# Optimization experiments

Measured on AMD Instinct MI355X. Metric: run time of the kernel, lower is better.

Reference implementation:

```python
import jax, jax.numpy as jnp
import numpy as np


def dct_mat(N, dtype=jnp.float32):
    # Orthonormal DCT-II matrix M: X = M @ x matches scipy dct(norm='ortho').
    n = jnp.arange(N, dtype=dtype)
    k = n[:, None]
    M = jnp.cos(jnp.pi * (2.0 * n[None, :] + 1.0) * k / (2.0 * N)) * jnp.sqrt(2.0 / N)
    M = M.at[0].multiply(1.0 / jnp.sqrt(2.0))
    return M


def setup_inputs() -> dict:
    key = jax.random.key(0)
    k1, k2, k3 = jax.random.split(key, 3)
    B, C, H, W = 8, 128, 200, 480  # H = 5*W/12 required by the slice/reshape logic
    x = jax.random.normal(k1, (B, C, H, W), dtype=jnp.float32)
    # nn.Linear(input_dim, input_dim//4, bias=False) weight: [C//4, C]
    w1 = jax.random.normal(k2, (C // 4, C), dtype=jnp.float32) * (1.0 / np.sqrt(C))
    # nn.Linear(input_dim//4, input_dim, bias=False) weight: [C, C//4]
    w2 = jax.random.normal(k3, (C, C // 4), dtype=jnp.float32) * (1.0 / np.sqrt(C // 4))
    return {"x": x, "w1": w1, "w2": w2}


def reference(x, w1, w2):
    LOW_W, HIGH_W = 0.6, 0.4
    B, C, H, W = x.shape
    D = dct_mat(W, x.dtype)
    # DCT-II (ortho) along the last (width) axis
    x_dct = jnp.einsum('bchn,kn->bchk', x, D)
    sp1, sp2 = W // 2, W // 4  # split points from x_dct.shape[-1]
    hs = H - sp2               # high-freq start index (uses height!)
    low = x_dct[:, :, :sp1, :sp1]                     # [B,C,min(H,sp1),sp1]
    high = x_dct[:, :, hs:, hs:].reshape(B, C, low.shape[2], low.shape[3])
    bal = LOW_W * low + HIGH_W * high
    # IDCT (DCT-III, ortho) along the last axis of the balanced spectrum
    D2 = dct_mat(low.shape[3], x.dtype)
    x_bal = jnp.einsum('bchk,kn->bchn', bal, D2)
    gap = jnp.mean(x_bal, axis=(2, 3))                # [B,C]
    att = jax.nn.sigmoid((gap @ w1.T) @ w2.T)         # SE-style channel gate
    return x * att[:, :, None, None]
```

## Files before the change

### kernel.cpp

```cpp
#include <hip/hip_runtime.h>
#include <math.h>


namespace {

constexpr int Hh     = 200;
constexpr int Ww     = 480;
constexpr int PLANE  = Hh * Ww;
constexpr int NBC    = 8 * 128;
constexpr int ROW4   = Ww / 4;
constexpr int CHUNK4 = (PLANE / 4) / 4;

__global__ __launch_bounds__(256) void gap_kernel(const float* __restrict__ x,
                                                  float* __restrict__ gap) {
    __shared__ float Wt[3][Ww];
    __shared__ float redp[4], redq[4];
    const int t = threadIdx.x;

    const float s   = 0.06454972243679028f;
    const float c2a = (float)(M_PI / 960.0);
    for (int n = t; n < Ww; n += 256) {
        int tn = 2 * n + 1;
        float a80  = (float)((tn * 80)  % 1920) * c2a;
        float a160 = (float)((tn * 160) % 1920) * c2a;
        float a240 = (float)((tn * 240) % 1920) * c2a;
        float a320 = (float)((tn * 320) % 1920) * c2a;
        float a400 = (float)((tn * 400) % 1920) * c2a;
        Wt[0][n] = s * (__cosf(a80)  + __cosf(a320));
        Wt[1][n] = s * (__cosf(a160) + __cosf(a400));
        Wt[2][n] = s * __cosf(a240);
    }
    __syncthreads();

    const int wave = t >> 6, lane = t & 63;
    const float4* xp = (const float4*)(x + (size_t)blockIdx.x * PLANE);
    float p = 0.f, q = 0.f;
    for (int h = wave; h < Hh; h += 4) {
        const float4* row = xp + h * ROW4;
        float4 v = row[lane];
        p += (v.x + v.y) + (v.z + v.w);
        float4 v2;
        const bool has2 = (lane < ROW4 - 64);
        if (has2) {
            v2 = row[lane + 64];
            p += (v2.x + v2.y) + (v2.z + v2.w);
        }
        if (h >= 80) {
            const float4* wrow = (const float4*)Wt[(h - 80) % 3];
            float4 wv = wrow[lane];
            q += v.x * wv.x + v.y * wv.y + v.z * wv.z + v.w * wv.w;
            if (has2) {
                float4 wv2 = wrow[lane + 64];
                q += v2.x * wv2.x + v2.y * wv2.y + v2.z * wv2.z + v2.w * wv2.w;
            }
        }
    }
    #pragma unroll
    for (int o = 32; o > 0; o >>= 1) {
        p += __shfl_down(p, o);
        q += __shfl_down(q, o);
    }
    if (lane == 0) { redp[wave] = p; redq[wave] = q; }
    __syncthreads();
    if (t == 0) {
        float P = (redp[0] + redp[1]) + (redp[2] + redp[3]);
        float Q = (redq[0] + redq[1]) + (redq[2] + redq[3]);
        float total = 0.02738612787525831f * P + 0.4f * Q;
        gap[blockIdx.x] = total * 3.227486121839514e-4f;
    }
}

__global__ __launch_bounds__(256) void att_kernel(const float* __restrict__ gap,
                                                  const float* __restrict__ w1,
                                                  const float* __restrict__ w2,
                                                  float* __restrict__ att) {
    __shared__ float g[1024];
    __shared__ float t1[8][32];
    const int t = threadIdx.x;
    for (int i = t; i < 1024; i += 256) g[i] = gap[i];
    __syncthreads();
    {
        const int b = t >> 5, j = t & 31;
        float acc = 0.f;
        #pragma unroll 8
        for (int c = 0; c < 128; c++) acc += g[b * 128 + c] * w1[j * 128 + c];
        t1[b][j] = acc;
    }
    __syncthreads();
    for (int i = t; i < 1024; i += 256) {
        const int b = i >> 7, c = i & 127;
        float acc = 0.f;
        #pragma unroll
        for (int j = 0; j < 32; j++) acc += t1[b][j] * w2[c * 32 + j];
        att[i] = 1.f / (1.f + __expf(-acc));
    }
}

__global__ __launch_bounds__(256) void scale_kernel(const float* __restrict__ x,
                                                    const float* __restrict__ att,
                                                    float* __restrict__ out) {
    const int bc = blockIdx.x;
    const float a = att[bc];
    const float4* xp = (const float4*)(x + (size_t)bc * PLANE);
    float4*       op = (float4*)(out + (size_t)bc * PLANE);
    const int start = blockIdx.y * CHUNK4;
    const int end   = start + CHUNK4;
    for (int i = start + threadIdx.x; i < end; i += 256) {
        float4 v = xp[i];
        v.x *= a; v.y *= a; v.z *= a; v.w *= a;
        op[i] = v;
    }
}

}

extern "C" void kernel_launch(void* const* d_in, const int* in_sizes, int n_in,
                              void* d_out, int out_size, void* d_ws, size_t ws_size,
                              hipStream_t stream) {
    const float* x  = (const float*)d_in[0];
    const float* w1 = (const float*)d_in[1];
    const float* w2 = (const float*)d_in[2];
    float* out = (float*)d_out;
    float* gap = (float*)d_ws;
    float* att = gap + 1024;

    gap_kernel<<<NBC, 256, 0, stream>>>(x, gap);
    att_kernel<<<1, 256, 0, stream>>>(gap, w1, w2, att);
    scale_kernel<<<dim3(NBC, 4), 256, 0, stream>>>(x, att, out);
}
```

Baseline: 733.9 us.

## Split GAP reduction across two blocks per plane, unroll rows, reverse scale order

The GAP kernel now uses two blocks per (b,c) plane, each covering 100 rows with a branchless 4-row unrolled loop, and writes partial (P,Q) sums. A zero weight row stands in for rows below 80. The attention kernel runs one block per batch and combines the two partials. The scale kernel walks planes in reverse order so it starts on data most recently read and possibly still in cache, and unrolls its loads four-wide. The aim is more parallelism and memory-level overlap in the reduction plus some cache reuse, at the cost of extra loads of zero weights for the first 80 rows.

```diff
diff --git a/kernel.cpp b/kernel.cpp
--- a/kernel.cpp
+++ b/kernel.cpp
@@ -4,16 +4,15 @@
 
 namespace {
 
-constexpr int Hh     = 200;
-constexpr int Ww     = 480;
-constexpr int PLANE  = Hh * Ww;
-constexpr int NBC    = 8 * 128;
-constexpr int ROW4   = Ww / 4;
-constexpr int CHUNK4 = (PLANE / 4) / 4;
+constexpr int Hh    = 200;
+constexpr int Ww    = 480;
+constexpr int PLANE = Hh * Ww;
+constexpr int NBC   = 8 * 128;
+constexpr int ROW4  = Ww / 4;
 
-__global__ __launch_bounds__(256) void gap_kernel(const float* __restrict__ x,
-                                                  float* __restrict__ gap) {
-    __shared__ float Wt[3][Ww];
+__global__ __launch_bounds__(256, 4) void gap_kernel(const float* __restrict__ x,
+                                                     float2* __restrict__ pq) {
+    __shared__ __align__(16) float Wt[4][Ww];
     __shared__ float redp[4], redq[4];
     const int t = threadIdx.x;
 
@@ -21,40 +20,54 @@
     const float c2a = (float)(M_PI / 960.0);
     for (int n = t; n < Ww; n += 256) {
         int tn = 2 * n + 1;
-        float a80  = (float)((tn * 80)  % 1920) * c2a;
-        float a160 = (float)((tn * 160) % 1920) * c2a;
-        float a240 = (float)((tn * 240) % 1920) * c2a;
-        float a320 = (float)((tn * 320) % 1920) * c2a;
-        float a400 = (float)((tn * 400) % 1920) * c2a;
-        Wt[0][n] = s * (__cosf(a80)  + __cosf(a320));
-        Wt[1][n] = s * (__cosf(a160) + __cosf(a400));
-        Wt[2][n] = s * __cosf(a240);
+        Wt[0][n] = s * (__cosf((float)((tn *  80) % 1920) * c2a) +
+                        __cosf((float)((tn * 320) % 1920) * c2a));
+        Wt[1][n] = s * (__cosf((float)((tn * 160) % 1920) * c2a) +
+                        __cosf((float)((tn * 400) % 1920) * c2a));
+        Wt[2][n] = s *  __cosf((float)((tn * 240) % 1920) * c2a);
+        Wt[3][n] = 0.f;
     }
     __syncthreads();
 
     const int wave = t >> 6, lane = t & 63;
-    const float4* xp = (const float4*)(x + (size_t)blockIdx.x * PLANE);
+    const int bc = blockIdx.x >> 1, part = blockIdx.x & 1;
+    const int r0 = part * 100;
+    const float4* xp = (const float4*)(x + (size_t)bc * PLANE);
+    const bool has2 = lane < (ROW4 - 64);
+    const float4 z4 = {0.f, 0.f, 0.f, 0.f};
+
     float p = 0.f, q = 0.f;
-    for (int h = wave; h < Hh; h += 4) {
-        const float4* row = xp + h * ROW4;
-        float4 v = row[lane];
-        p += (v.x + v.y) + (v.z + v.w);
-        float4 v2;
-        const bool has2 = (lane < ROW4 - 64);
-        if (has2) {
-            v2 = row[lane + 64];
-            p += (v2.x + v2.y) + (v2.z + v2.w);
-        }
-        if (h >= 80) {
-            const float4* wrow = (const float4*)Wt[(h - 80) % 3];
-            float4 wv = wrow[lane];
-            q += v.x * wv.x + v.y * wv.y + v.z * wv.z + v.w * wv.w;
-            if (has2) {
-                float4 wv2 = wrow[lane + 64];
-                q += v2.x * wv2.x + v2.y * wv2.y + v2.z * wv2.z + v2.w * wv2.w;
-            }
+    for (int tile = 0; tile < 6; tile++) {
+        const int hb = r0 + tile * 16 + wave * 4;
+        #pragma unroll
+        for (int rr = 0; rr < 4; rr++) {
+            const int h = hb + rr;
+            const float4* row = xp + h * ROW4;
+            float4 v  = row[lane];
+            float4 v2 = has2 ? row[lane + 64] : z4;
+            const int cls = (h < 80) ? 3 : (h - 80) % 3;
+            const float4* wrow = (const float4*)Wt[cls];
+            float4 wv  = wrow[lane];
+            float4 wv2 = has2 ? wrow[lane + 64] : z4;
+            p += (v.x + v.y) + (v.z + v.w) + (v2.x + v2.y) + (v2.z + v2.w);
+            q += v.x * wv.x + v.y * wv.y + v.z * wv.z + v.w * wv.w
+               + v2.x * wv2.x + v2.y * wv2.y + v2.z * wv2.z + v2.w * wv2.w;
         }
     }
+    {
+        const int h = r0 + 96 + wave;
+        const float4* row = xp + h * ROW4;
+        float4 v  = row[lane];
+        float4 v2 = has2 ? row[lane + 64] : z4;
+        const int cls = (h < 80) ? 3 : (h - 80) % 3;
+        const float4* wrow = (const float4*)Wt[cls];
+        float4 wv  = wrow[lane];
+        float4 wv2 = has2 ? wrow[lane + 64] : z4;
+        p += (v.x + v.y) + (v.z + v.w) + (v2.x + v2.y) + (v2.z + v2.w);
+        q += v.x * wv.x + v.y * wv.y + v.z * wv.z + v.w * wv.w
+           + v2.x * wv2.x + v2.y * wv2.y + v2.z * wv2.z + v2.w * wv2.w;
+    }
+
     #pragma unroll
     for (int o = 32; o > 0; o >>= 1) {
         p += __shfl_down(p, o);
@@ -65,47 +78,58 @@
     if (t == 0) {
         float P = (redp[0] + redp[1]) + (redp[2] + redp[3]);
         float Q = (redq[0] + redq[1]) + (redq[2] + redq[3]);
-        float total = 0.02738612787525831f * P + 0.4f * Q;
-        gap[blockIdx.x] = total * 3.227486121839514e-4f;
+        pq[blockIdx.x] = make_float2(P, Q);
     }
 }
 
-__global__ __launch_bounds__(256) void att_kernel(const float* __restrict__ gap,
+__global__ __launch_bounds__(256) void att_kernel(const float2* __restrict__ pq,
                                                   const float* __restrict__ w1,
                                                   const float* __restrict__ w2,
                                                   float* __restrict__ att) {
-    __shared__ float g[1024];
-    __shared__ float t1[8][32];
-    const int t = threadIdx.x;
-    for (int i = t; i < 1024; i += 256) g[i] = gap[i];
-    __syncthreads();
-    {
-        const int b = t >> 5, j = t & 31;
-        float acc = 0.f;
-        #pragma unroll 8
-        for (int c = 0; c < 128; c++) acc += g[b * 128 + c] * w1[j * 128 + c];
-        t1[b][j] = acc;
+    __shared__ float g[128];
+    __shared__ float t1[32];
+    const int b = blockIdx.x, t = threadIdx.x;
+    if (t < 128) {
+        float2 a0 = pq[(b * 128 + t) * 2 + 0];
+        float2 a1 = pq[(b * 128 + t) * 2 + 1];
+        float P = a0.x + a1.x, Q = a0.y + a1.y;
+        g[t] = (0.02738612787525831f * P + 0.4f * Q) * 3.227486121839514e-4f;
     }
     __syncthreads();
-    for (int i = t; i < 1024; i += 256) {
-        const int b = i >> 7, c = i & 127;
+    if (t < 32) {
         float acc = 0.f;
         #pragma unroll
-        for (int j = 0; j < 32; j++) acc += t1[b][j] * w2[c * 32 + j];
-        att[i] = 1.f / (1.f + __expf(-acc));
+        for (int c = 0; c < 128; c++) acc += g[c] * w1[t * 128 + c];
+        t1[t] = acc;
+    }
+    __syncthreads();
+    if (t < 128) {
+        float acc = 0.f;
+        #pragma unroll
+        for (int j = 0; j < 32; j++) acc += t1[j] * w2[t * 32 + j];
+        att[b * 128 + t] = 1.f / (1.f + __expf(-acc));
     }
 }
 
 __global__ __launch_bounds__(256) void scale_kernel(const float* __restrict__ x,
                                                     const float* __restrict__ att,
                                                     float* __restrict__ out) {
-    const int bc = blockIdx.x;
+    const int bc = (NBC - 1) - (int)blockIdx.x;
     const float a = att[bc];
-    const float4* xp = (const float4*)(x + (size_t)bc * PLANE);
-    float4*       op = (float4*)(out + (size_t)bc * PLANE);
-    const int start = blockIdx.y * CHUNK4;
-    const int end   = start + CHUNK4;
-    for (int i = start + threadIdx.x; i < end; i += 256) {
+    const float4* __restrict__ xp = (const float4*)(x   + (size_t)bc * PLANE);
+    float4* __restrict__       op = (float4*)      (out + (size_t)bc * PLANE);
+    const int start = blockIdx.y * 6000;
+    const int end   = start + 6000;
+    int i = start + (int)threadIdx.x;
+    for (; i + 768 < end; i += 1024) {
+        float4 v0 = xp[i], v1 = xp[i + 256], v2 = xp[i + 512], v3 = xp[i + 768];
+        v0.x *= a; v0.y *= a; v0.z *= a; v0.w *= a;
+        v1.x *= a; v1.y *= a; v1.z *= a; v1.w *= a;
+        v2.x *= a; v2.y *= a; v2.z *= a; v2.w *= a;
+        v3.x *= a; v3.y *= a; v3.z *= a; v3.w *= a;
+        op[i] = v0; op[i + 256] = v1; op[i + 512] = v2; op[i + 768] = v3;
+    }
+    for (; i < end; i += 256) {
         float4 v = xp[i];
         v.x *= a; v.y *= a; v.z *= a; v.w *= a;
         op[i] = v;
@@ -121,10 +145,10 @@
     const float* w1 = (const float*)d_in[1];
     const float* w2 = (const float*)d_in[2];
     float* out = (float*)d_out;
-    float* gap = (float*)d_ws;
-    float* att = gap + 1024;
+    float2* pq = (float2*)d_ws;
+    float* att = (float*)d_ws + 4096;
 
-    gap_kernel<<<NBC, 256, 0, stream>>>(x, gap);
-    att_kernel<<<1, 256, 0, stream>>>(gap, w1, w2, att);
+    gap_kernel<<<NBC * 2, 256, 0, stream>>>(x, pq);
+    att_kernel<<<8, 256, 0, stream>>>(pq, w1, w2, att);
     scale_kernel<<<dim3(NBC, 4), 256, 0, stream>>>(x, att, out);
 }
```

After: 715.7 us. 2.5% less time.
